# Kernel tuning notes

Hardware: AMD Instinct MI355X
Metric: run time of the kernel (lower is better)

The kernel has to match this reference:

```python
import jax, jax.numpy as jnp
import numpy as np

B, S, E, H = 2, 2048, 1024, 16
HD = E // H

def setup_inputs() -> dict:
    key = jax.random.key(0)
    ks = jax.random.split(key, 12)
    q = jax.random.normal(ks[0], (B, S, E), jnp.float32)
    k = jax.random.normal(ks[1], (B, S, E), jnp.float32)
    v = jax.random.normal(ks[2], (B, S, E), jnp.float32)
    # causal mask: 1.0 where attention is disallowed (upper triangle)
    mask = jnp.triu(jnp.ones((S, S), jnp.float32), k=1)[None, None, :, :]
    w = lambda kk: jax.random.normal(kk, (E, E), jnp.float32) * 0.02
    return {
        "q": q, "k": k, "v": v, "mask": mask,
        "Wq": w(ks[3]), "bq": jnp.zeros((E,), jnp.float32),
        "Wk": w(ks[4]), "bk": jnp.zeros((E,), jnp.float32),
        "Wv": w(ks[5]), "bv": jnp.zeros((E,), jnp.float32),
        "Wz": w(ks[6]), "bz": jnp.zeros((E,), jnp.float32),
    }

def _create_heads(x):
    # Faithful to tf.reshape(tf.transpose(x), (B, H, -1, HD)):
    # tf.transpose reverses all dims: [B,S,E] -> [E,S,B], then reshape.
    return jnp.transpose(x, (2, 1, 0)).reshape(B, H, -1, HD)

def reference(q, k, v, mask, Wq, bq, Wk, bk, Wv, bv, Wz, bz):
    qh = _create_heads(q @ Wq + bq)  # (B,H,S,HD)
    kh = _create_heads(k @ Wk + bk)
    vh = _create_heads(v @ Wv + bv)
    qn = qh / jnp.linalg.norm(qh, axis=-1, keepdims=True)
    kn = kh / jnp.linalg.norm(kh, axis=-1, keepdims=True)
    logits = jnp.einsum('bhqd,bhkd->bhqk', qn, kn) * 1000.0
    logits = logits + mask * -1000000000.0
    attn = jax.nn.softmax(logits, axis=-1)  # (B,H,S,S)
    z = jnp.einsum('bhqk,bhkd->bhqd', attn, vh)
    zc = jnp.transpose(z, (0, 2, 1, 3)).reshape(B, -1, E)
    return zc @ Wz + bz, attn
```

## Files before the change

### kernel.cpp

```cpp
#include <hip/hip_runtime.h>
#include <cstdint>
#include <cstddef>


typedef __bf16 bf16x4 __attribute__((ext_vector_type(4)));
typedef __bf16 bf16x8 __attribute__((ext_vector_type(8)));
typedef float floatx4 __attribute__((ext_vector_type(4)));

#define GLOAD_LDS16(g, l)                                                      \
    __builtin_amdgcn_global_load_lds(                                          \
        (const __attribute__((address_space(1))) void*)(g),                    \
        (__attribute__((address_space(3))) void*)(l), 16, 0, 0)

__device__ __forceinline__ void nt_store4(float* p, floatx4 v) {
    __builtin_nontemporal_store(v, (floatx4*)p);
}

__global__ __launch_bounds__(256) void prep(
    const float* __restrict__ x0, const float* __restrict__ x1,
    const float* __restrict__ x2, __bf16* __restrict__ ApBase,
    const float* __restrict__ w0, const float* __restrict__ w1,
    const float* __restrict__ w2, const float* __restrict__ w3,
    __bf16* __restrict__ Bp0, __bf16* __restrict__ BpzDst, int nW)
{
    const int flat = (int)blockIdx.x;
    const int tid = (int)threadIdx.x;

    if (flat < 12288) {
        const int z = flat >> 12;
        const int bx = flat & 4095;
        const float* X = z == 0 ? x0 : (z == 1 ? x1 : x2);
        __bf16* Ap = ApBase + (size_t)z * (4096ull * 2048);
        const int idx = bx * 256 + tid;
        const int r = idx >> 8;
        const int c = (idx & 255) * 4;
        float4 t = *(const float4*)(X + (size_t)r * 1024 + c);
        bf16x4 hi, lo;
        hi[0] = (__bf16)t.x; lo[0] = (__bf16)(t.x - (float)hi[0]);
        hi[1] = (__bf16)t.y; lo[1] = (__bf16)(t.y - (float)hi[1]);
        hi[2] = (__bf16)t.z; lo[2] = (__bf16)(t.z - (float)hi[2]);
        hi[3] = (__bf16)t.w; lo[3] = (__bf16)(t.w - (float)hi[3]);
        *(bf16x4*)(Ap + (size_t)r * 2048 + c) = hi;
        *(bf16x4*)(Ap + (size_t)r * 2048 + 1024 + c) = lo;
        return;
    }

    const int t = flat - 12288;
    const int slice = t >> 8;
    if (slice >= nW) return;
    const int idx = t & 255;
    const float* W = slice == 0 ? w0 : (slice == 1 ? w1 : (slice == 2 ? w2 : w3));
    __bf16* Bp = slice < 3 ? (Bp0 + (size_t)slice * (1024ull * 2048)) : BpzDst;

    __shared__ float tile[64][65];
    const int k0 = (idx >> 4) * 64, n0 = (idx & 15) * 64;
    #pragma unroll
    for (int p = 0; p < 4; ++p) {
        int kr = p * 16 + (tid >> 4);
        float4 v = *(const float4*)(W + (size_t)(k0 + kr) * 1024 + n0 + (tid & 15) * 4);
        tile[kr][(tid & 15) * 4 + 0] = v.x; tile[kr][(tid & 15) * 4 + 1] = v.y;
        tile[kr][(tid & 15) * 4 + 2] = v.z; tile[kr][(tid & 15) * 4 + 3] = v.w;
    }
    __syncthreads();
    const int nr = tid >> 2, kc = (tid & 3) * 16;
    bf16x8 hi0, hi1, lo0, lo1;
    #pragma unroll
    for (int j = 0; j < 8; ++j) {
        float x = tile[kc + j][nr];
        __bf16 h = (__bf16)x; hi0[j] = h; lo0[j] = (__bf16)(x - (float)h);
        float y = tile[kc + 8 + j][nr];
        __bf16 g = (__bf16)y; hi1[j] = g; lo1[j] = (__bf16)(y - (float)g);
    }
    __bf16* row = Bp + (size_t)(n0 + nr) * 2048;
    *(bf16x8*)(row + k0 + kc)            = hi0;
    *(bf16x8*)(row + k0 + kc + 8)        = hi1;
    *(bf16x8*)(row + 1024 + k0 + kc)     = lo0;
    *(bf16x8*)(row + 1024 + k0 + kc + 8) = lo1;
}

__global__ __launch_bounds__(256) void split_bt1(
    const float* __restrict__ W, __bf16* __restrict__ Bp)
{
    __shared__ float tile[64][65];
    const int tid = (int)threadIdx.x;
    const int k0 = blockIdx.y * 64, n0 = blockIdx.x * 64;
    #pragma unroll
    for (int p = 0; p < 4; ++p) {
        int kr = p * 16 + (tid >> 4);
        float4 v = *(const float4*)(W + (size_t)(k0 + kr) * 1024 + n0 + (tid & 15) * 4);
        tile[kr][(tid & 15) * 4 + 0] = v.x; tile[kr][(tid & 15) * 4 + 1] = v.y;
        tile[kr][(tid & 15) * 4 + 2] = v.z; tile[kr][(tid & 15) * 4 + 3] = v.w;
    }
    __syncthreads();
    const int nr = tid >> 2, kc = (tid & 3) * 16;
    bf16x8 hi0, hi1, lo0, lo1;
    #pragma unroll
    for (int j = 0; j < 8; ++j) {
        float x = tile[kc + j][nr];
        __bf16 h = (__bf16)x; hi0[j] = h; lo0[j] = (__bf16)(x - (float)h);
        float y = tile[kc + 8 + j][nr];
        __bf16 g = (__bf16)y; hi1[j] = g; lo1[j] = (__bf16)(y - (float)g);
    }
    __bf16* row = Bp + (size_t)(n0 + nr) * 2048;
    *(bf16x8*)(row + k0 + kc)            = hi0;
    *(bf16x8*)(row + k0 + kc + 8)        = hi1;
    *(bf16x8*)(row + 1024 + k0 + kc)     = lo0;
    *(bf16x8*)(row + 1024 + k0 + kc + 8) = lo1;
}

__global__ __launch_bounds__(256) void gemm_split(
    const __bf16* __restrict__ Ap0, size_t aSlice, int aStride,
    const __bf16* __restrict__ Bp0, size_t bSlice,
    const float* __restrict__ b0, const float* __restrict__ b1,
    const float* __restrict__ b2, float* __restrict__ Out0,
    int transposeOut, int chunksQK, int chunksV,
    __bf16* __restrict__ Qp, __bf16* __restrict__ Kp, int fuseQK)
{
    const int z = blockIdx.z;
    const int nch = (z == 2) ? chunksV : chunksQK;
    const bool fuse = fuseQK && (z < 2);
    const __bf16* Ap = Ap0 + (size_t)z * aSlice;
    const __bf16* Bp = Bp0 + (size_t)z * bSlice;
    const float* bias = z == 0 ? b0 : (z == 1 ? b1 : b2);
    float* Out = Out0 + (size_t)z * (4096ull * 1024);

    __shared__ __bf16 As[2 * 128 * 32];
    __shared__ __bf16 Bs[2 * 128 * 32];

    const int tid = (int)threadIdx.x;
    const int wave = tid >> 6, lane = tid & 63;
    const int quad = lane >> 4, tl = lane & 15;
    const int m0 = blockIdx.y * 128, n0 = blockIdx.x * 128;
    const int waveM = wave >> 1, waveN = wave & 1;

    floatx4 acc[4][4];
    #pragma unroll
    for (int i = 0; i < 4; ++i)
        #pragma unroll
        for (int j = 0; j < 4; ++j)
            acc[i][j] = (floatx4){0.f, 0.f, 0.f, 0.f};

    const int sRow  = (wave << 4) + (lane >> 2);
    const int sColB = (lane & 3) << 4;
    auto* AsL = (__attribute__((address_space(3))) char*)As;
    auto* BsL = (__attribute__((address_space(3))) char*)Bs;
    const int ldsOff = wave * 1024;

    size_t aRow[2];
    #pragma unroll
    for (int i = 0; i < 2; ++i) {
        const int mrow = i * 64 + sRow;
        if (fuse) {
            const int u = mrow & 63;
            aRow[i] = (size_t)((u >> 5) * 2048 + (m0 >> 1) + (mrow >> 6) * 32 + (u & 31));
        } else {
            aRow[i] = (size_t)(m0 + mrow);
        }
    }

    for (int k0 = 0; k0 < 1024; k0 += 32) {
        __syncthreads();
        #pragma unroll
        for (int i = 0; i < 2; ++i) {
            GLOAD_LDS16((const char*)(Ap + aRow[i] * aStride + k0) + sColB,
                        AsL + i * 4096 + ldsOff);
            GLOAD_LDS16((const char*)(Bp + (size_t)(n0 + i*64 + sRow) * 2048 + k0) + sColB,
                        BsL + i * 4096 + ldsOff);
            if (nch > 1) {
                GLOAD_LDS16((const char*)(Ap + 1024 + aRow[i] * aStride + k0) + sColB,
                            AsL + 8192 + i * 4096 + ldsOff);
                GLOAD_LDS16((const char*)(Bp + 1024 + (size_t)(n0 + i*64 + sRow) * 2048 + k0) + sColB,
                            BsL + 8192 + i * 4096 + ldsOff);
            }
        }
        __syncthreads();

        bf16x8 ah[4], bh[4], al[4], bl[4];
        #pragma unroll
        for (int mt = 0; mt < 4; ++mt)
            ah[mt] = *(const bf16x8*)(As + (waveM*64 + mt*16 + tl) * 32 + quad * 8);
        #pragma unroll
        for (int nt = 0; nt < 4; ++nt)
            bh[nt] = *(const bf16x8*)(Bs + (waveN*64 + nt*16 + tl) * 32 + quad * 8);
        #pragma unroll
        for (int mt = 0; mt < 4; ++mt)
            #pragma unroll
            for (int nt = 0; nt < 4; ++nt)
                acc[mt][nt] = __builtin_amdgcn_mfma_f32_16x16x32_bf16(
                    ah[mt], bh[nt], acc[mt][nt], 0, 0, 0);
        if (nch > 1) {
            #pragma unroll
            for (int mt = 0; mt < 4; ++mt)
                al[mt] = *(const bf16x8*)(As + 4096 + (waveM*64 + mt*16 + tl) * 32 + quad * 8);
            #pragma unroll
            for (int mt = 0; mt < 4; ++mt)
                #pragma unroll
                for (int nt = 0; nt < 4; ++nt)
                    acc[mt][nt] = __builtin_amdgcn_mfma_f32_16x16x32_bf16(
                        al[mt], bh[nt], acc[mt][nt], 0, 0, 0);
        }
        if (nch > 2) {
            #pragma unroll
            for (int nt = 0; nt < 4; ++nt)
                bl[nt] = *(const bf16x8*)(Bs + 4096 + (waveN*64 + nt*16 + tl) * 32 + quad * 8);
            #pragma unroll
            for (int mt = 0; mt < 4; ++mt)
                #pragma unroll
                for (int nt = 0; nt < 4; ++nt)
                    acc[mt][nt] = __builtin_amdgcn_mfma_f32_16x16x32_bf16(
                        ah[mt], bl[nt], acc[mt][nt], 0, 0, 0);
        }
    }

    if (fuse) {
        __bf16* Outp = (z == 0) ? Qp : Kp;
        const int g = ((m0 >> 7) << 1) + waveM;
        #pragma unroll
        for (int nt = 0; nt < 4; ++nt) {
            const int e = n0 + waveN * 64 + nt * 16 + tl;
            const float bb = bias[e];
            float vals[16];
            float ss = 0.f;
            #pragma unroll
            for (int mt = 0; mt < 4; ++mt)
                #pragma unroll
                for (int reg = 0; reg < 4; ++reg) {
                    float vv = acc[mt][nt][reg] + bb;
                    vals[mt * 4 + reg] = vv;
                    ss += vv * vv;
                }
            ss += __shfl_xor(ss, 16);
            ss += __shfl_xor(ss, 32);
            const float inv = 1.0f / sqrtf(ss);
            const int head = ((e >> 9) << 4) + ((e >> 5) & 15);
            const int sp = ((e & 31) << 6) + g;
            __bf16* row = Outp + ((size_t)head * 2048 + sp) * 128;
            #pragma unroll
            for (int mt = 0; mt < 4; ++mt)
                #pragma unroll
                for (int reg = 0; reg < 4; ++reg) {
                    const int u = mt * 16 + quad * 4 + reg;
                    const int d = ((u & 31) << 1) | (u >> 5);
                    float vv = vals[mt * 4 + reg] * inv;
                    __bf16 h = (__bf16)vv;
                    row[d] = h;
                    row[64 + d] = (__bf16)(vv - (float)h);
                }
        }
    } else if (transposeOut) {
        #pragma unroll
        for (int nt = 0; nt < 4; ++nt) {
            const int e = n0 + waveN * 64 + nt * 16 + tl;
            const float bb = bias[e];
            #pragma unroll
            for (int mt = 0; mt < 4; ++mt) {
                floatx4 v = acc[mt][nt] + bb;
                *(floatx4*)(Out + (size_t)e * 4096 + m0 + waveM * 64 + mt * 16 + quad * 4) = v;
            }
        }
    } else {
        #pragma unroll
        for (int mt = 0; mt < 4; ++mt) {
            const int rbase = m0 + waveM * 64 + mt * 16 + quad * 4;
            #pragma unroll
            for (int nt = 0; nt < 4; ++nt) {
                const int e = n0 + waveN * 64 + nt * 16 + tl;
                const float bb = bias[e];
                #pragma unroll
                for (int reg = 0; reg < 4; ++reg)
                    Out[(size_t)(rbase + reg) * 1024 + e] = acc[mt][nt][reg] + bb;
            }
        }
    }
}

__global__ __launch_bounds__(256) void v_transpose(
    const float* __restrict__ PT0, __bf16* __restrict__ Vt)
{
    const int t = (int)blockIdx.x;
    const int tid = (int)threadIdx.x;
    const int st = t & 31, head = t >> 5;
    const float* PTv = PT0 + 8388608;
    const int c = (head >> 4) * 512 + (head & 15) * 32 + st;
    const float* __restrict__ row = PTv + (size_t)c * 4096;

    __shared__ float tile[64][65];
    #pragma unroll
    for (int i = 0; i < 4; ++i) {
        int o = i * 1024 + tid * 4;
        float4 v4 = *(const float4*)(row + o);
        float vals[4] = {v4.x, v4.y, v4.z, v4.w};
        #pragma unroll
        for (int e = 0; e < 4; ++e) {
            int oo = o + e;
            int d  = ((oo & 2047) & 31) * 2 + (oo >> 11);
            int sl = (oo & 2047) >> 5;
            tile[sl][d] = vals[e];
        }
    }
    __syncthreads();

    const int d = tid >> 2, jb = (tid & 3) * 16;
    bf16x8 h0, h1;
    #pragma unroll
    for (int j = 0; j < 8; ++j) {
        h0[j] = (__bf16)tile[jb + j][d];
        h1[j] = (__bf16)tile[jb + 8 + j][d];
    }
    size_t bh = ((size_t)head * 64 + d) * 2048 + st * 64 + jb;
    *(bf16x8*)(Vt + bh)     = h0;
    *(bf16x8*)(Vt + bh + 8) = h1;
}

__global__ __launch_bounds__(512, 4) void attn_mfma(
    const __bf16* __restrict__ Qp, const __bf16* __restrict__ Kp,
    const __bf16* __restrict__ Vt, float* __restrict__ Attn,
    __bf16* __restrict__ Az)
{
    const int flat = (int)blockIdx.x;
    const int head = flat & 31;
    const int idx  = flat >> 5;
    const int it   = (idx < 8) ? (15 - idx) : (idx - 8);
    const int tid = (int)threadIdx.x;
    const int w = tid >> 6, lane = tid & 63;
    const int quad = lane >> 4, tl = lane & 15;
    const int t7 = tl & 7;
    const int i0 = it * 128;
    const int jtmax = 2 * it + 1;
    const int wrowMax = i0 + w * 16 + 15;
    const int wdiag   = (i0 + w * 16) >> 6;
    const int irowBase = w * 16 + quad * 4;

    const __bf16* __restrict__ Qh = Qp + ((size_t)head * 2048 + i0) * 128;
    const __bf16* __restrict__ Kh = Kp + (size_t)head * 2048 * 128;
    const __bf16* __restrict__ Vh = Vt + (size_t)head * 64 * 2048;
    float* __restrict__ Ah = Attn + (size_t)head * ((size_t)2048 * 2048);

    __shared__ __bf16 kb[2][64 * 128];
    __shared__ __bf16 vt[2][64 * 64];
    __shared__ __bf16 ps[8][16 * 72];
    __bf16* psw = ps[w];
    auto* kbL = (__attribute__((address_space(3))) char*)&kb[0][0];
    auto* vtL = (__attribute__((address_space(3))) char*)&vt[0][0];

    const char* kSrc[2];
    #pragma unroll
    for (int i = 0; i < 2; ++i) {
        int d  = i * 512 + tid;
        int rK = d >> 4, cK = (d & 15) ^ (rK & 7);
        kSrc[i] = (const char*)(Kh + (size_t)rK * 128) + cK * 16;
    }
    const char* vSrc;
    {
        int rV = tid >> 3, cV = (tid & 7) ^ (rV & 7);
        vSrc = (const char*)(Vh + (size_t)rV * 2048) + cV * 16;
    }
    const int ok0 = ((quad)      ^ t7) * 8;
    const int ok1 = ((quad + 4)  ^ t7) * 8;
    const int ok2 = ((quad + 8)  ^ t7) * 8;
    const int ok3 = ((quad + 12) ^ t7) * 8;

    const __bf16* qrow = Qh + (size_t)(w * 16 + tl) * 128;
    bf16x8 qhi0 = *(const bf16x8*)(qrow + quad * 8);
    bf16x8 qhi1 = *(const bf16x8*)(qrow + 32 + quad * 8);
    bf16x8 qlo0 = *(const bf16x8*)(qrow + 64 + quad * 8);
    bf16x8 qlo1 = *(const bf16x8*)(qrow + 96 + quad * 8);

    for (int jt = jtmax + 1; jt < 32; ++jt) {
        floatx4 z4 = (floatx4){0.f, 0.f, 0.f, 0.f};
        #pragma unroll
        for (int g = 0; g < 4; ++g)
            nt_store4(Ah + (size_t)(i0 + w * 16 + g * 4 + quad) * 2048
                          + jt * 64 + tl * 4, z4);
    }

    float m[4], l[4];
    #pragma unroll
    for (int r = 0; r < 4; ++r) { m[r] = -3.0e38f; l[r] = 0.0f; }

    #pragma unroll
    for (int i = 0; i < 2; ++i)
        GLOAD_LDS16(kSrc[i], kbL + i * 8192 + w * 1024);

    for (int jt = 0; jt <= jtmax; ++jt) {
        const int cur = jt & 1;
        __syncthreads();
        if (jt < jtmax) {
            #pragma unroll
            for (int i = 0; i < 2; ++i)
                GLOAD_LDS16(kSrc[i] + (size_t)(jt + 1) * 16384,
                            kbL + (cur ^ 1) * 16384 + i * 8192 + w * 1024);
        }
        if (jt * 64 > wrowMax) continue;

        const __bf16* kbuf = &kb[cur][0];
        const bool diag = (jt == wdiag);
        #pragma unroll
        for (int sub = 0; sub < 4; ++sub) {
            const __bf16* kr = kbuf + (sub * 16 + tl) * 128;
            bf16x8 khi0 = *(const bf16x8*)(kr + ok0);
            bf16x8 khi1 = *(const bf16x8*)(kr + ok1);
            bf16x8 klo0 = *(const bf16x8*)(kr + ok2);
            bf16x8 klo1 = *(const bf16x8*)(kr + ok3);
            floatx4 s = (floatx4){0.f, 0.f, 0.f, 0.f};
            s = __builtin_amdgcn_mfma_f32_16x16x32_bf16(qhi0, khi0, s, 0, 0, 0);
            s = __builtin_amdgcn_mfma_f32_16x16x32_bf16(qhi1, khi1, s, 0, 0, 0);
            s = __builtin_amdgcn_mfma_f32_16x16x32_bf16(qhi0, klo0, s, 0, 0, 0);
            s = __builtin_amdgcn_mfma_f32_16x16x32_bf16(qhi1, klo1, s, 0, 0, 0);
            s = __builtin_amdgcn_mfma_f32_16x16x32_bf16(qlo0, khi0, s, 0, 0, 0);
            s = __builtin_amdgcn_mfma_f32_16x16x32_bf16(qlo1, khi1, s, 0, 0, 0);
            const int col = jt * 64 + sub * 16 + tl;
            #pragma unroll
            for (int reg = 0; reg < 4; ++reg) {
                float lv = s[reg] * 1000.0f;
                if (diag && (col > i0 + irowBase + reg)) lv = -1.0e9f;
                float mn = fmaxf(m[reg], lv);
                l[reg] = l[reg] * __expf(m[reg] - mn) + __expf(lv - mn);
                m[reg] = mn;
            }
        }
    }

    #pragma unroll
    for (int reg = 0; reg < 4; ++reg) {
        #pragma unroll
        for (int mk = 8; mk >= 1; mk >>= 1) {
            float mo = __shfl_xor(m[reg], mk);
            float lo = __shfl_xor(l[reg], mk);
            float mn = fmaxf(m[reg], mo);
            l[reg] = l[reg] * __expf(m[reg] - mn) + lo * __expf(mo - mn);
            m[reg] = mn;
        }
    }
    float inv_l[4];
    #pragma unroll
    for (int reg = 0; reg < 4; ++reg) inv_l[reg] = 1.0f / l[reg];

    floatx4 zacc[4];
    #pragma unroll
    for (int t = 0; t < 4; ++t) zacc[t] = (floatx4){0.f, 0.f, 0.f, 0.f};

    #pragma unroll
    for (int i = 0; i < 2; ++i)
        GLOAD_LDS16(kSrc[i], kbL + i * 8192 + w * 1024);
    GLOAD_LDS16(vSrc, vtL + w * 1024);

    for (int jt = 0; jt <= jtmax; ++jt) {
        const int cur = jt & 1;
        __syncthreads();
        if (jt < jtmax) {
            #pragma unroll
            for (int i = 0; i < 2; ++i)
                GLOAD_LDS16(kSrc[i] + (size_t)(jt + 1) * 16384,
                            kbL + (cur ^ 1) * 16384 + i * 8192 + w * 1024);
            GLOAD_LDS16(vSrc + (size_t)(jt + 1) * 128,
                        vtL + (cur ^ 1) * 8192 + w * 1024);
        }

        if (jt * 64 > wrowMax) {
            floatx4 z4 = (floatx4){0.f, 0.f, 0.f, 0.f};
            #pragma unroll
            for (int g = 0; g < 4; ++g)
                nt_store4(Ah + (size_t)(i0 + w * 16 + g * 4 + quad) * 2048
                              + jt * 64 + tl * 4, z4);
            continue;
        }

        const __bf16* kbuf = &kb[cur][0];
        const __bf16* vbuf = &vt[cur][0];
        const bool diag = (jt == wdiag);
        #pragma unroll
        for (int sub = 0; sub < 4; ++sub) {
            const __bf16* kr = kbuf + (sub * 16 + tl) * 128;
            bf16x8 khi0 = *(const bf16x8*)(kr + ok0);
            bf16x8 khi1 = *(const bf16x8*)(kr + ok1);
            bf16x8 klo0 = *(const bf16x8*)(kr + ok2);
            bf16x8 klo1 = *(const bf16x8*)(kr + ok3);
            floatx4 s = (floatx4){0.f, 0.f, 0.f, 0.f};
            s = __builtin_amdgcn_mfma_f32_16x16x32_bf16(qhi0, khi0, s, 0, 0, 0);
            s = __builtin_amdgcn_mfma_f32_16x16x32_bf16(qhi1, khi1, s, 0, 0, 0);
            s = __builtin_amdgcn_mfma_f32_16x16x32_bf16(qhi0, klo0, s, 0, 0, 0);
            s = __builtin_amdgcn_mfma_f32_16x16x32_bf16(qhi1, klo1, s, 0, 0, 0);
            s = __builtin_amdgcn_mfma_f32_16x16x32_bf16(qlo0, khi0, s, 0, 0, 0);
            s = __builtin_amdgcn_mfma_f32_16x16x32_bf16(qlo1, khi1, s, 0, 0, 0);
            const int col = jt * 64 + sub * 16 + tl;
            #pragma unroll
            for (int reg = 0; reg < 4; ++reg) {
                float lv = s[reg] * 1000.0f;
                if (diag && (col > i0 + irowBase + reg)) lv = -1.0e9f;
                float p = __expf(lv - m[reg]) * inv_l[reg];
                psw[(quad * 4 + reg) * 72 + sub * 16 + tl] = (__bf16)p;
            }
        }
        __asm__ volatile("s_waitcnt lgkmcnt(0)" ::: "memory");

        #pragma unroll
        for (int g = 0; g < 4; ++g) {
            bf16x4 pv = *(const bf16x4*)(psw + (g * 4 + quad) * 72 + tl * 4);
            floatx4 f = (floatx4){(float)pv[0], (float)pv[1],
                                  (float)pv[2], (float)pv[3]};
            nt_store4(Ah + (size_t)(i0 + w * 16 + g * 4 + quad) * 2048
                          + jt * 64 + tl * 4, f);
        }

        bf16x8 p0 = *(const bf16x8*)(psw + tl * 72 + quad * 8);
        bf16x8 p1 = *(const bf16x8*)(psw + tl * 72 + 32 + quad * 8);
        #pragma unroll
        for (int t = 0; t < 4; ++t) {
            const __bf16* vh0 = vbuf + (t * 16 + tl) * 64;
            bf16x8 vhi0 = *(const bf16x8*)(vh0 + ok0);
            bf16x8 vhi1 = *(const bf16x8*)(vh0 + ok1);
            zacc[t] = __builtin_amdgcn_mfma_f32_16x16x32_bf16(p0, vhi0, zacc[t], 0, 0, 0);
            zacc[t] = __builtin_amdgcn_mfma_f32_16x16x32_bf16(p1, vhi1, zacc[t], 0, 0, 0);
        }
    }

    const int b = head >> 4, h = head & 15;
    #pragma unroll
    for (int reg = 0; reg < 4; ++reg) {
        const size_t R = (size_t)b * 2048 + i0 + w * 16 + quad * 4 + reg;
        #pragma unroll
        for (int t = 0; t < 4; ++t)
            Az[R * 1024 + h * 64 + t * 16 + tl] = (__bf16)zacc[t][reg];
    }
}

extern "C" void kernel_launch(void* const* d_in, const int* in_sizes, int n_in,
                              void* d_out, int out_size, void* d_ws, size_t ws_size,
                              hipStream_t stream) {
    (void)in_sizes; (void)n_in; (void)out_size;
    const float* q  = (const float*)d_in[0];
    const float* k  = (const float*)d_in[1];
    const float* v  = (const float*)d_in[2];
    const float* Wq = (const float*)d_in[4];  const float* bq = (const float*)d_in[5];
    const float* Wk = (const float*)d_in[6];  const float* bk = (const float*)d_in[7];
    const float* Wv = (const float*)d_in[8];  const float* bv = (const float*)d_in[9];
    const float* Wz = (const float*)d_in[10]; const float* bz = (const float*)d_in[11];

    float* out0 = (float*)d_out;
    float* attn = out0 + 4194304;

    float*  PT0 = attn;
    __bf16* Ap0 = (__bf16*)(attn + 12582912);
    __bf16* Bp0 = (__bf16*)(attn + 12582912 + 12582912);

    __bf16 *Qp, *Kp, *Vtp, *Az, *Bpz;
    const bool bigWs = ws_size >= (size_t)54525952;
    if (bigWs) {
        __bf16* ws = (__bf16*)d_ws;
        Qp = ws; Kp = ws + 8388608; Vtp = ws + 16777216; Az = ws + 20971520;
        Bpz = ws + 25165824;
    } else {
        Qp = (__bf16*)d_in[0]; Kp = (__bf16*)d_in[1]; Vtp = (__bf16*)d_in[2];
        Az = (__bf16*)d_ws;
        Bpz = (__bf16*)d_in[4];
    }

    if (bigWs) {
        prep<<<dim3(12288 + 4 * 256), 256, 0, stream>>>(
            q, k, v, Ap0, Wq, Wk, Wv, Wz, Bp0, Bpz, 4);
    } else {
        prep<<<dim3(12288 + 3 * 256), 256, 0, stream>>>(
            q, k, v, Ap0, Wq, Wk, Wv, Wz, Bp0, nullptr, 3);
        split_bt1<<<dim3(16, 16), 256, 0, stream>>>(Wz, Bpz);
    }

    gemm_split<<<dim3(8, 32, 3), 256, 0, stream>>>(
        Ap0, 4096ull*2048, 2048, Bp0, 1024ull*2048,
        bq, bk, bv, PT0, 1, 3, 1,
        Qp, Kp, 1);

    v_transpose<<<dim3(1024), 256, 0, stream>>>(PT0, Vtp);

    attn_mfma<<<dim3(512), 512, 0, stream>>>(Qp, Kp, Vtp, attn, Az);

    gemm_split<<<dim3(8, 32, 1), 256, 0, stream>>>(
        Az, 0, 1024, Bpz, 0,
        bz, bz, bz, out0, 0, 1, 1,
        nullptr, nullptr, 0);
}
```

Measured before the change: 807.6 us.

## Use exp2 softmax with folded log2e, swap GEMM grid order, vectorize Q/K stores

The attention softmax folds log2(e) into the 1000x logit scale and uses exp2f in place of __expf, removing a multiply per exponential. The GEMM block mapping swaps blockIdx.x/y so consecutive blocks walk along M rather than N, which changes L2 reuse of the weight tiles. The normalized Q/K hi/lo epilogue now packs four bf16 values per vector store instead of scalar stores. The -1e9 mask sentinel stays in the scaled domain, so the masked values are unchanged in effect.

```diff
diff --git a/kernel.cpp b/kernel.cpp
--- a/kernel.cpp
+++ b/kernel.cpp
@@ -15,6 +15,8 @@
 __device__ __forceinline__ void nt_store4(float* p, floatx4 v) {
     __builtin_nontemporal_store(v, (floatx4*)p);
 }
+
+#define LOG2E_1000 1442.6950408889634f
 
 __global__ __launch_bounds__(256) void prep(
     const float* __restrict__ x0, const float* __restrict__ x1,
@@ -130,7 +132,7 @@
     const int tid = (int)threadIdx.x;
     const int wave = tid >> 6, lane = tid & 63;
     const int quad = lane >> 4, tl = lane & 15;
-    const int m0 = blockIdx.y * 128, n0 = blockIdx.x * 128;
+    const int m0 = blockIdx.x * 128, n0 = blockIdx.y * 128;
     const int waveM = wave >> 1, waveN = wave & 1;
 
     floatx4 acc[4][4];
@@ -236,15 +238,21 @@
             const int sp = ((e & 31) << 6) + g;
             __bf16* row = Outp + ((size_t)head * 2048 + sp) * 128;
             #pragma unroll
-            for (int mt = 0; mt < 4; ++mt)
+            for (int mt = 0; mt < 2; ++mt)
                 #pragma unroll
-                for (int reg = 0; reg < 4; ++reg) {
-                    const int u = mt * 16 + quad * 4 + reg;
-                    const int d = ((u & 31) << 1) | (u >> 5);
-                    float vv = vals[mt * 4 + reg] * inv;
-                    __bf16 h = (__bf16)vv;
-                    row[d] = h;
-                    row[64 + d] = (__bf16)(vv - (float)h);
+                for (int r0 = 0; r0 < 4; r0 += 2) {
+                    const int d0 = (mt * 16 + quad * 4 + r0) * 2;
+                    float v0 = vals[mt * 4 + r0] * inv;
+                    float v1 = vals[(mt + 2) * 4 + r0] * inv;
+                    float v2 = vals[mt * 4 + r0 + 1] * inv;
+                    float v3 = vals[(mt + 2) * 4 + r0 + 1] * inv;
+                    bf16x4 hv, lo4;
+                    hv[0] = (__bf16)v0; lo4[0] = (__bf16)(v0 - (float)hv[0]);
+                    hv[1] = (__bf16)v1; lo4[1] = (__bf16)(v1 - (float)hv[1]);
+                    hv[2] = (__bf16)v2; lo4[2] = (__bf16)(v2 - (float)hv[2]);
+                    hv[3] = (__bf16)v3; lo4[3] = (__bf16)(v3 - (float)hv[3]);
+                    *(bf16x4*)(row + d0) = hv;
+                    *(bf16x4*)(row + 64 + d0) = lo4;
                 }
         }
     } else if (transposeOut) {
@@ -412,10 +420,10 @@
             const int col = jt * 64 + sub * 16 + tl;
             #pragma unroll
             for (int reg = 0; reg < 4; ++reg) {
-                float lv = s[reg] * 1000.0f;
+                float lv = s[reg] * LOG2E_1000;
                 if (diag && (col > i0 + irowBase + reg)) lv = -1.0e9f;
                 float mn = fmaxf(m[reg], lv);
-                l[reg] = l[reg] * __expf(m[reg] - mn) + __expf(lv - mn);
+                l[reg] = l[reg] * exp2f(m[reg] - mn) + exp2f(lv - mn);
                 m[reg] = mn;
             }
         }
@@ -428,7 +436,7 @@
             float mo = __shfl_xor(m[reg], mk);
             float lo = __shfl_xor(l[reg], mk);
             float mn = fmaxf(m[reg], mo);
-            l[reg] = l[reg] * __expf(m[reg] - mn) + lo * __expf(mo - mn);
+            l[reg] = l[reg] * exp2f(m[reg] - mn) + lo * exp2f(mo - mn);
             m[reg] = mn;
         }
     }
@@ -486,9 +494,9 @@
             const int col = jt * 64 + sub * 16 + tl;
             #pragma unroll
             for (int reg = 0; reg < 4; ++reg) {
-                float lv = s[reg] * 1000.0f;
+                float lv = s[reg] * LOG2E_1000;
                 if (diag && (col > i0 + irowBase + reg)) lv = -1.0e9f;
-                float p = __expf(lv - m[reg]) * inv_l[reg];
+                float p = exp2f(lv - m[reg]) * inv_l[reg];
                 psw[(quad * 4 + reg) * 72 + sub * 16 + tl] = (__bf16)p;
             }
         }
@@ -565,7 +573,7 @@
         split_bt1<<<dim3(16, 16), 256, 0, stream>>>(Wz, Bpz);
     }
 
-    gemm_split<<<dim3(8, 32, 3), 256, 0, stream>>>(
+    gemm_split<<<dim3(32, 8, 3), 256, 0, stream>>>(
         Ap0, 4096ull*2048, 2048, Bp0, 1024ull*2048,
         bq, bk, bv, PT0, 1, 3, 1,
         Qp, Kp, 1);
@@ -574,7 +582,7 @@
 
     attn_mfma<<<dim3(512), 512, 0, stream>>>(Qp, Kp, Vtp, attn, Az);
 
-    gemm_split<<<dim3(8, 32, 1), 256, 0, stream>>>(
+    gemm_split<<<dim3(32, 8, 1), 256, 0, stream>>>(
         Az, 0, 1024, Bpz, 0,
         bz, bz, bz, out0, 0, 1, 1,
         nullptr, nullptr, 0);
```

Result: no change. 823.6 us (+2.0%).
